# Kernel tuning notes

Hardware: AMD Instinct MI355X
Metric: run time of the kernel (lower is better)

Reference implementation:

```python
import jax, jax.numpy as jnp
import numpy as np

B, S, D, H = 16, 1024, 768, 12
HD = D // H
SCALE = HD ** -0.5


def setup_inputs() -> dict:
    key = jax.random.key(0)
    k1, k2, k3, k4 = jax.random.split(key, 4)
    # Xavier-uniform-like init for the linear weights
    lim_qkv = (6.0 / (D + 3 * D)) ** 0.5
    lim_proj = (6.0 / (D + D)) ** 0.5
    return {
        "hidden_states": jax.random.normal(k1, (B, S, D), dtype=jnp.float32),
        "mask": jax.random.randint(k2, (B, S), 0, 2).astype(bool),
        "qkv_w": jax.random.uniform(k3, (3 * D, D), minval=-lim_qkv, maxval=lim_qkv, dtype=jnp.float32),
        "qkv_b": jnp.zeros((3 * D,), dtype=jnp.float32),
        "proj_w": jax.random.uniform(k4, (D, D), minval=-lim_proj, maxval=lim_proj, dtype=jnp.float32),
        "proj_b": jnp.zeros((D,), dtype=jnp.float32),
    }


def _masked_softmax(scores, attn_mask):
    # scores: [B,H,S,S]; attn_mask: [B,1,S,S] bool. Fully-masked rows -> all-zero
    # weights (torch gives NaN there but then zeroes the output rows; zeroing
    # the weights yields the identical final output without NaNs).
    neg_inf = jnp.finfo(scores.dtype).min
    m = jnp.max(jnp.where(attn_mask, scores, neg_inf), axis=-1, keepdims=True)
    e = jnp.where(attn_mask, jnp.exp(scores - m), 0.0)
    denom = jnp.sum(e, axis=-1, keepdims=True)
    return e / jnp.where(denom == 0, 1.0, denom)


def reference(hidden_states, mask, qkv_w, qkv_b, proj_w, proj_b):
    # fused QKV projection: [B,S,3D]
    qkv = hidden_states @ qkv_w.T + qkv_b
    qkv = qkv.reshape(B, S, 3, H, HD).transpose(2, 0, 3, 1, 4)  # [3,B,H,S,hd]
    q, k, v = qkv[0], qkv[1], qkv[2]
    tok_mask = mask[:, None, :, None]  # [B,1,S,1]
    q = jnp.where(tok_mask, q, 0.0)
    k = jnp.where(tok_mask, k, 0.0)
    v = jnp.where(tok_mask, v, 0.0)
    scores = jnp.einsum("bhqd,bhkd->bhqk", q, k) * SCALE
    attn_mask = (mask[:, :, None] & mask[:, None, :])[:, None]  # [B,1,S,S]
    attn = _masked_softmax(scores, attn_mask)
    context = jnp.einsum("bhqk,bhkd->bhqd", attn, v)
    context = context.transpose(0, 2, 1, 3).reshape(B, S, D)
    out = context @ proj_w.T + proj_b
    out = jnp.where(mask[:, :, None], out, 0.0)
    return out
```

## Files before the change

### kernel.cpp

```cpp
#include <hip/hip_runtime.h>
#include <cstdint>
#include <cstddef>

#define B 16
#define S 1024
#define D 768
#define H 12
#define HD 64
#define NTOK (B * S)
#define QKV_N (3 * D)
#define SCALE 0.125f
#define C2 2.88539008f
#define GK 768
#define NT_K 12

typedef _Float16 f16x8 __attribute__((ext_vector_type(8)));
typedef _Float16 f16x4 __attribute__((ext_vector_type(4)));
typedef __fp16 fp16x2 __attribute__((ext_vector_type(2)));
typedef float f32x4 __attribute__((ext_vector_type(4)));

typedef __attribute__((address_space(3))) void as3_void;
typedef const __attribute__((address_space(1))) void as1_void;

#if defined(__has_builtin)
#if __has_builtin(__builtin_amdgcn_exp2f)
#define EXP2(x) __builtin_amdgcn_exp2f(x)
#else
#define EXP2(x) exp2f(x)
#endif
#else
#define EXP2(x) exp2f(x)
#endif

__global__ __launch_bounds__(256) void normalize_mask_kernel(
    const unsigned char* __restrict__ raw, int* __restrict__ outm, int n) {
    __shared__ int s_isbyte;
    const int tid = threadIdx.x;
    if (tid == 0) s_isbyte = 0;
    __syncthreads();
    int found = 0;
    for (int i = tid; i < n; i += 256) {
        if ((i & 3) != 0 && raw[i] != 0) found = 1;
    }
    if (found) atomicOr(&s_isbyte, 1);
    __syncthreads();
    const int isbyte = s_isbyte;
    if (isbyte) {
        for (int i = tid; i < n; i += 256) outm[i] = raw[i] ? 1 : 0;
    } else {
        const int* r32 = (const int*)raw;
        for (int i = tid; i < n; i += 256) outm[i] = r32[i] ? 1 : 0;
    }
}

__global__ __launch_bounds__(256) void cvt_all_f16(
    const float* __restrict__ in0, _Float16* __restrict__ out0, int n0,
    const float* __restrict__ in1, _Float16* __restrict__ out1, int n1,
    const float* __restrict__ in2, _Float16* __restrict__ out2, int n2) {
    int i = blockIdx.x * 256 + threadIdx.x;
    const float* in;
    _Float16* out;
    if (i < n0) { in = in0; out = out0; }
    else if (i < n0 + n1) { i -= n0; in = in1; out = out1; }
    else { i -= n0 + n1; in = in2; out = out2; if (i >= n2) return; }
    const float4 v = ((const float4*)in)[i];
    f16x4 o;
    o[0] = (_Float16)v.x; o[1] = (_Float16)v.y;
    o[2] = (_Float16)v.z; o[3] = (_Float16)v.w;
    ((f16x4*)out)[i] = o;
}

template <int MODE>
__global__ __launch_bounds__(256, 2) void gemm16(
    const _Float16* __restrict__ A, const _Float16* __restrict__ Wm,
    const float* __restrict__ bias, const int* __restrict__ rowmask,
    int N, float* __restrict__ outf, _Float16* __restrict__ outh,
    _Float16* __restrict__ vtb) {
    __shared__ _Float16 smem[32768];

    const int tid = threadIdx.x;
    const int w = tid >> 6, l = tid & 63;
    const int wm = (w >> 1) * 64, wn = (w & 1) * 64;
    const int lg = l >> 4, lc = l & 15;

    const int bid = blockIdx.x;
    const int xcd = bid & 7;
    const int idx = bid >> 3;
    const int bn = (idx >> 4) * 128;
    const int bm = (xcd * 16 + (idx & 15)) * 128;

    f32x4 acc[4][4] = {};

#define STAGE(T, BUF)                                                           \
    {                                                                           \
        const int kt_ = (T) * 64;                                               \
        _Pragma("unroll")                                                       \
        for (int i_ = 0; i_ < 4; ++i_) {                                        \
            const int ci_ = (w << 2) + i_;                           \
            const int r_ = (ci_ << 3) + (l >> 3);                               \
            const int c16_ = (l & 7) ^ (r_ & 7);                                \
            __builtin_amdgcn_global_load_lds(                                   \
                (as1_void*)(A + (size_t)(bm + r_) * GK + kt_ + c16_ * 8),       \
                (as3_void*)(smem + (BUF) * 8192 + ci_ * 512), 16, 0, 0);        \
            __builtin_amdgcn_global_load_lds(                                   \
                (as1_void*)(Wm + (size_t)(bn + r_) * GK + kt_ + c16_ * 8),      \
                (as3_void*)(smem + 16384 + (BUF) * 8192 + ci_ * 512), 16, 0, 0);\
        }                                                                       \
    }

    STAGE(0, 0)

    for (int t = 0; t < NT_K; ++t) {
        const int cur = t & 1;
        if (t + 1 < NT_K) {
            STAGE(t + 1, cur ^ 1)
            asm volatile("s_waitcnt vmcnt(8)" ::: "memory");
        } else {
            asm volatile("s_waitcnt vmcnt(0)" ::: "memory");
        }
        __builtin_amdgcn_s_barrier();

        const _Float16* sA = smem + cur * 8192;
        const _Float16* sB = smem + 16384 + cur * 8192;
        __builtin_amdgcn_s_setprio(1);
#pragma unroll
        for (int kk = 0; kk < 2; ++kk) {
            const int c16 = ((kk << 2) + lg) ^ (lc & 7);
            f16x8 af[4], bf[4];
#pragma unroll
            for (int ni = 0; ni < 4; ++ni)
                bf[ni] = *(const f16x8*)&sB[(wn + ni * 16 + lc) * 64 + c16 * 8];
#pragma unroll
            for (int mi = 0; mi < 4; ++mi)
                af[mi] = *(const f16x8*)&sA[(wm + mi * 16 + lc) * 64 + c16 * 8];
#pragma unroll
            for (int mi = 0; mi < 4; ++mi)
#pragma unroll
                for (int ni = 0; ni < 4; ++ni)
                    acc[mi][ni] = __builtin_amdgcn_mfma_f32_16x16x32_f16(
                        af[mi], bf[ni], acc[mi][ni], 0, 0, 0);
        }
        __builtin_amdgcn_s_setprio(0);
        __builtin_amdgcn_s_barrier();
    }
#undef STAGE

    float bs[4];
#pragma unroll
    for (int ni = 0; ni < 4; ++ni) bs[ni] = bias[bn + wn + ni * 16 + lc];

    if (MODE == 1) {
        if (bn < 1536) {
#pragma unroll
            for (int mi = 0; mi < 4; ++mi) {
#pragma unroll
                for (int j = 0; j < 4; ++j) {
                    const int m = bm + wm + mi * 16 + lg * 4 + j;
#pragma unroll
                    for (int ni = 0; ni < 4; ++ni) {
                        const int col = bn + wn + ni * 16 + lc;
                        outh[(size_t)m * N + col] =
                            (_Float16)(acc[mi][ni][j] + bs[ni]);
                    }
                }
            }
        } else {
#pragma unroll
            for (int mi = 0; mi < 4; ++mi) {
#pragma unroll
                for (int ni = 0; ni < 4; ++ni) {
                    f16x4 v4;
#pragma unroll
                    for (int j = 0; j < 4; ++j)
                        v4[j] = (_Float16)(acc[mi][ni][j] + bs[ni]);
                    const int nl = wn + ni * 16 + lc;
                    const int ml = wm + mi * 16 + lg * 4;
                    *(f16x4*)&smem[nl * 136 + ml] = v4;
                }
            }
            __syncthreads();
            const int r = tid >> 1;
            const int c0 = (tid & 1) * 64;
            const int col0 = bn - 1536 + r;
            const int hh = col0 >> 6, hd = col0 & 63;
            const int bb = bm >> 10;
            const int s0 = (bm & 1023) + c0;
            _Float16* dst = vtb + ((size_t)(bb * H + hh) * HD + hd) * S + s0;
#pragma unroll
            for (int e = 0; e < 8; ++e)
                *(f16x8*)(dst + e * 8) = *(const f16x8*)&smem[r * 136 + c0 + e * 8];
        }
    } else {
#pragma unroll
        for (int mi = 0; mi < 4; ++mi) {
#pragma unroll
            for (int j = 0; j < 4; ++j) {
                const int m = bm + wm + mi * 16 + lg * 4 + j;
                const int mv = rowmask[m];
#pragma unroll
                for (int ni = 0; ni < 4; ++ni) {
                    const int col = bn + wn + ni * 16 + lc;
                    outf[(size_t)m * N + col] = mv ? acc[mi][ni][j] + bs[ni] : 0.f;
                }
            }
        }
    }
}

__global__ __launch_bounds__(256) void attn_kernel(
    const _Float16* __restrict__ qkv, const _Float16* __restrict__ vtb,
    const int* __restrict__ mask, _Float16* __restrict__ ctx) {
    __shared__ _Float16 ksm[2][64 * 64];
    __shared__ _Float16 vsm[2][64 * 68];
    __shared__ float mbias[S];

    const int blk = blockIdx.x;
    const int xcd = blk & 7;
    const int idx = blk >> 3;
    const int bh_ = xcd * 24 + (idx >> 3);
    const int qt = idx & 7;
    const int h = bh_ % H;
    const int b = bh_ / H;
    const int tid = threadIdx.x;
    const int w = tid >> 6, lane = tid & 63;
    const int lg = lane >> 4, lc = lane & 15;

    const size_t bh = (size_t)(b * H + h);
    const _Float16* Kp = qkv + (size_t)(b * S) * QKV_N + D + h * HD;
    const _Float16* Vt = vtb + bh * HD * S;
    const int* mrow = mask + b * S;

    const int r0 = w * 8 + (lane >> 3);
    const int s0 = lane & 7;
    const int koff0 = r0 * QKV_N + (s0 ^ (r0 & 7)) * 8;
    const int koff1 = (32 + r0) * QKV_N + (s0 ^ ((32 + r0) & 7)) * 8;
    const int srow = tid >> 3;
    const int scol = (tid & 7) * 8;

#define KSTAGE(KT, BUF)                                                        \
    {                                                                          \
        __builtin_amdgcn_global_load_lds(                                      \
            (as1_void*)(Kp + (size_t)(KT) * QKV_N + koff0),                    \
            (as3_void*)(&ksm[BUF][w * 512]), 16, 0, 0);                        \
        __builtin_amdgcn_global_load_lds(                                      \
            (as1_void*)(Kp + (size_t)(KT) * QKV_N + koff1),                    \
            (as3_void*)(&ksm[BUF][2048 + w * 512]), 16, 0, 0);                 \
    }

    const int qrow0 = qt * 128 + w * 16 + lc;
    const _Float16* Qp0 = qkv + (size_t)(b * S + qrow0) * QKV_N + h * HD;
    const _Float16* Qp1 = Qp0 + (size_t)64 * QKV_N;
    f16x8 qa0 = *(const f16x8*)(Qp0 + lg * 8);
    f16x8 qa1 = *(const f16x8*)(Qp0 + 32 + lg * 8);
    f16x8 qb0 = *(const f16x8*)(Qp1 + lg * 8);
    f16x8 qb1 = *(const f16x8*)(Qp1 + 32 + lg * 8);
    const _Float16 qs = (_Float16)(0.125f * 1.44269504f);
    qa0 *= qs; qa1 *= qs; qb0 *= qs; qb1 *= qs;

#pragma unroll
    for (int i = 0; i < 4; ++i)
        mbias[i * 256 + tid] = mrow[i * 256 + tid] ? -C2 : -1e9f;

    KSTAGE(0, 0)
    {
        const f16x8 gv0 = *(const f16x8*)(Vt + (size_t)srow * S + scol);
        const f16x8 gv1 = *(const f16x8*)(Vt + (size_t)(32 + srow) * S + scol);
        asm volatile("s_waitcnt vmcnt(0)" ::: "memory");
        *(f16x4*)&vsm[0][srow * 68 + scol] = ((const f16x4*)&gv0)[0];
        *(f16x4*)&vsm[0][srow * 68 + scol + 4] = ((const f16x4*)&gv0)[1];
        *(f16x4*)&vsm[0][(32 + srow) * 68 + scol] = ((const f16x4*)&gv1)[0];
        *(f16x4*)&vsm[0][(32 + srow) * 68 + scol + 4] = ((const f16x4*)&gv1)[1];
    }
    __syncthreads();

    f32x4 acca[4] = {}, accb[4] = {};
    float l_a = 0.f, l_b = 0.f;
    fp16x2 ones;
    ones[0] = (__fp16)1.0f; ones[1] = (__fp16)1.0f;

    for (int it = 0; it < S / 64; ++it) {
        const int cur = it & 1;
        const int ktn = (it + 1) * 64;
        const bool pref = (it + 1 < S / 64);
        f16x8 gv0, gv1;
        if (pref) {
            KSTAGE(ktn, cur ^ 1)
            gv0 = *(const f16x8*)(Vt + (size_t)srow * S + ktn + scol);
            gv1 = *(const f16x8*)(Vt + (size_t)(32 + srow) * S + ktn + scol);
        }

        __builtin_amdgcn_s_setprio(1);
#pragma unroll
        for (int t = 0; t < 4; ++t) {
            const int krow = (t * 16 + lc) * 64;
            const f16x8 kfa =
                *(const f16x8*)&ksm[cur][krow + (lg ^ (lc & 7)) * 8];
            const f16x8 kfb =
                *(const f16x8*)&ksm[cur][krow + ((4 + lg) ^ (lc & 7)) * 8];
            const f32x4 mb = *(const f32x4*)&mbias[it * 64 + t * 16 + 4 * lg];

            f32x4 ca = mb, cb = mb;
            ca = __builtin_amdgcn_mfma_f32_16x16x32_f16(kfa, qa0, ca, 0, 0, 0);
            ca = __builtin_amdgcn_mfma_f32_16x16x32_f16(kfb, qa1, ca, 0, 0, 0);
            cb = __builtin_amdgcn_mfma_f32_16x16x32_f16(kfa, qb0, cb, 0, 0, 0);
            cb = __builtin_amdgcn_mfma_f32_16x16x32_f16(kfb, qb1, cb, 0, 0, 0);

            const auto ua0 = __builtin_amdgcn_cvt_pkrtz(EXP2(ca[0]), EXP2(ca[1]));
            const auto ua1 = __builtin_amdgcn_cvt_pkrtz(EXP2(ca[2]), EXP2(ca[3]));
            const auto ub0 = __builtin_amdgcn_cvt_pkrtz(EXP2(cb[0]), EXP2(cb[1]));
            const auto ub1 = __builtin_amdgcn_cvt_pkrtz(EXP2(cb[2]), EXP2(cb[3]));
            l_a = __builtin_amdgcn_fdot2(ua0, ones, l_a, false);
            l_a = __builtin_amdgcn_fdot2(ua1, ones, l_a, false);
            l_b = __builtin_amdgcn_fdot2(ub0, ones, l_b, false);
            l_b = __builtin_amdgcn_fdot2(ub1, ones, l_b, false);

            f16x4 pa, pb;
            pa[0] = (_Float16)ua0[0]; pa[1] = (_Float16)ua0[1];
            pa[2] = (_Float16)ua1[0]; pa[3] = (_Float16)ua1[1];
            pb[0] = (_Float16)ub0[0]; pb[1] = (_Float16)ub0[1];
            pb[2] = (_Float16)ub1[0]; pb[3] = (_Float16)ub1[1];

#pragma unroll
            for (int g = 0; g < 4; ++g) {
                const f16x4 vf =
                    *(const f16x4*)&vsm[cur][(g * 16 + lc) * 68 + t * 16 + lg * 4];
                acca[g] = __builtin_amdgcn_mfma_f32_16x16x16f16(pa, vf, acca[g], 0, 0, 0);
                accb[g] = __builtin_amdgcn_mfma_f32_16x16x16f16(pb, vf, accb[g], 0, 0, 0);
            }
        }
        __builtin_amdgcn_s_setprio(0);

        if (pref) {
            asm volatile("s_waitcnt vmcnt(0)" ::: "memory");
            *(f16x4*)&vsm[cur ^ 1][srow * 68 + scol] = ((const f16x4*)&gv0)[0];
            *(f16x4*)&vsm[cur ^ 1][srow * 68 + scol + 4] = ((const f16x4*)&gv0)[1];
            *(f16x4*)&vsm[cur ^ 1][(32 + srow) * 68 + scol] = ((const f16x4*)&gv1)[0];
            *(f16x4*)&vsm[cur ^ 1][(32 + srow) * 68 + scol + 4] = ((const f16x4*)&gv1)[1];
        }
        __syncthreads();
    }
#undef KSTAGE

    float la = l_a, lb = l_b;
    la += __shfl_xor(la, 16); la += __shfl_xor(la, 32);
    lb += __shfl_xor(lb, 16); lb += __shfl_xor(lb, 32);
    const float inva = la > 0.f ? 1.f / la : 0.f;
    const float invb = lb > 0.f ? 1.f / lb : 0.f;

#pragma unroll
    for (int j = 0; j < 4; ++j) {
        const int qin = 4 * lg + j;
        const float ija = __shfl(inva, qin);
        const float ijb = __shfl(invb, qin);
        const int qra = qt * 128 + w * 16 + qin;
        const int qrb = qra + 64;
        const float iqa = mrow[qra] ? ija : 0.f;
        const float iqb = mrow[qrb] ? ijb : 0.f;
        const size_t oa = ((size_t)(b * S + qra)) * D + h * HD;
        const size_t ob = ((size_t)(b * S + qrb)) * D + h * HD;
#pragma unroll
        for (int g = 0; g < 4; ++g) {
            ctx[oa + 16 * g + lc] = (_Float16)(acca[g][j] * iqa);
            ctx[ob + 16 * g + lc] = (_Float16)(accb[g][j] * iqb);
        }
    }
}

extern "C" void kernel_launch(void* const* d_in, const int* in_sizes, int n_in,
                              void* d_out, int out_size, void* d_ws, size_t ws_size,
                              hipStream_t stream) {
    const float* hidden = (const float*)d_in[0];
    const unsigned char* maskraw = (const unsigned char*)d_in[1];
    const float* qkv_w = (const float*)d_in[2];
    const float* qkv_b = (const float*)d_in[3];
    const float* proj_w = (const float*)d_in[4];
    const float* proj_b = (const float*)d_in[5];
    float* out = (float*)d_out;

    char* ws = (char*)d_ws;
    size_t off = 0;
    int* maskN = (int*)(ws + off);            off += (size_t)NTOK * 4;
    _Float16* hid16 = (_Float16*)(ws + off);  off += (size_t)NTOK * D * 2;
    _Float16* qkvw16 = (_Float16*)(ws + off); off += (size_t)QKV_N * D * 2;
    _Float16* projw16 = (_Float16*)(ws + off); off += (size_t)D * D * 2;
    _Float16* qkv16 = (_Float16*)(ws + off);  off += (size_t)NTOK * QKV_N * 2;
    _Float16* vt = (_Float16*)(ws + off);     off += (size_t)NTOK * D * 2;
    _Float16* ctx16 = (_Float16*)(ws + off);  off += (size_t)NTOK * D * 2;

    normalize_mask_kernel<<<1, 256, 0, stream>>>(maskraw, maskN, NTOK);

    const int n0 = NTOK * D / 4, n1 = QKV_N * D / 4, n2 = D * D / 4;
    cvt_all_f16<<<(n0 + n1 + n2 + 255) / 256, 256, 0, stream>>>(
        hidden, hid16, n0, qkv_w, qkvw16, n1, proj_w, projw16, n2);

    gemm16<1><<<dim3(2304), 256, 0, stream>>>(
        hid16, qkvw16, qkv_b, nullptr, QKV_N, nullptr, qkv16, vt);

    attn_kernel<<<dim3(B * H * (S / 128)), 256, 0, stream>>>(qkv16, vt, maskN, ctx16);

    gemm16<0><<<dim3(768), 256, 0, stream>>>(
        ctx16, projw16, proj_b, maskN, D, out, nullptr, nullptr);
}
```

Measured before the change: 207.7 us.

## Double attention query tile per block and stage V via async LDS loads

Each attention block now handles 256 query rows (4 groups of 64 per wave set) instead of 128, so every K/V tile loaded into shared memory is reused across twice as many queries and the grid halves. V tiles are now staged with global_load_lds directly into an XOR-swizzled 64-wide layout, like K, replacing register round-trips, the padded 68 stride and the explicit vmcnt wait. Launch bounds request 3 blocks per CU, which raises register pressure given the larger accumulator set (16 f32x4 accumulators plus 8 Q fragments) and risks spills or lower occupancy. Fewer blocks (768) may also reduce load balance across CUs.

```diff
diff --git a/kernel.cpp b/kernel.cpp
--- a/kernel.cpp
+++ b/kernel.cpp
@@ -207,18 +207,18 @@
     }
 }
 
-__global__ __launch_bounds__(256) void attn_kernel(
+__global__ __launch_bounds__(256, 3) void attn_kernel(
     const _Float16* __restrict__ qkv, const _Float16* __restrict__ vtb,
     const int* __restrict__ mask, _Float16* __restrict__ ctx) {
     __shared__ _Float16 ksm[2][64 * 64];
-    __shared__ _Float16 vsm[2][64 * 68];
+    __shared__ _Float16 vsm[2][64 * 64];
     __shared__ float mbias[S];
 
     const int blk = blockIdx.x;
     const int xcd = blk & 7;
     const int idx = blk >> 3;
-    const int bh_ = xcd * 24 + (idx >> 3);
-    const int qt = idx & 7;
+    const int bh_ = xcd * 24 + (idx >> 2);
+    const int qt = idx & 3;
     const int h = bh_ % H;
     const int b = bh_ / H;
     const int tid = threadIdx.x;
@@ -231,13 +231,13 @@
     const int* mrow = mask + b * S;
 
     const int r0 = w * 8 + (lane >> 3);
-    const int s0 = lane & 7;
-    const int koff0 = r0 * QKV_N + (s0 ^ (r0 & 7)) * 8;
-    const int koff1 = (32 + r0) * QKV_N + (s0 ^ ((32 + r0) & 7)) * 8;
-    const int srow = tid >> 3;
-    const int scol = (tid & 7) * 8;
-
-#define KSTAGE(KT, BUF)                                                        \
+    const int swz8 = ((lane & 7) ^ (r0 & 7)) * 8;
+    const int koff0 = r0 * QKV_N + swz8;
+    const int koff1 = (32 + r0) * QKV_N + swz8;
+    const int voff0 = r0 * S + swz8;
+    const int voff1 = (32 + r0) * S + swz8;
+
+#define STAGE(KT, BUF)                                                         \
     {                                                                          \
         __builtin_amdgcn_global_load_lds(                                      \
             (as1_void*)(Kp + (size_t)(KT) * QKV_N + koff0),                    \
@@ -245,49 +245,42 @@
         __builtin_amdgcn_global_load_lds(                                      \
             (as1_void*)(Kp + (size_t)(KT) * QKV_N + koff1),                    \
             (as3_void*)(&ksm[BUF][2048 + w * 512]), 16, 0, 0);                 \
-    }
-
-    const int qrow0 = qt * 128 + w * 16 + lc;
-    const _Float16* Qp0 = qkv + (size_t)(b * S + qrow0) * QKV_N + h * HD;
-    const _Float16* Qp1 = Qp0 + (size_t)64 * QKV_N;
-    f16x8 qa0 = *(const f16x8*)(Qp0 + lg * 8);
-    f16x8 qa1 = *(const f16x8*)(Qp0 + 32 + lg * 8);
-    f16x8 qb0 = *(const f16x8*)(Qp1 + lg * 8);
-    f16x8 qb1 = *(const f16x8*)(Qp1 + 32 + lg * 8);
+        __builtin_amdgcn_global_load_lds(                                      \
+            (as1_void*)(Vt + (size_t)(KT) + voff0),                            \
+            (as3_void*)(&vsm[BUF][w * 512]), 16, 0, 0);                        \
+        __builtin_amdgcn_global_load_lds(                                      \
+            (as1_void*)(Vt + (size_t)(KT) + voff1),                            \
+            (as3_void*)(&vsm[BUF][2048 + w * 512]), 16, 0, 0);                 \
+    }
+
+    const int qbase = qt * 256 + w * 16 + lc;
     const _Float16 qs = (_Float16)(0.125f * 1.44269504f);
-    qa0 *= qs; qa1 *= qs; qb0 *= qs; qb1 *= qs;
+    f16x8 qf[4][2];
+#pragma unroll
+    for (int qg = 0; qg < 4; ++qg) {
+        const _Float16* Qp =
+            qkv + (size_t)(b * S + qbase + qg * 64) * QKV_N + h * HD;
+        qf[qg][0] = *(const f16x8*)(Qp + lg * 8);
+        qf[qg][1] = *(const f16x8*)(Qp + 32 + lg * 8);
+        qf[qg][0] *= qs;
+        qf[qg][1] *= qs;
+    }
 
 #pragma unroll
     for (int i = 0; i < 4; ++i)
         mbias[i * 256 + tid] = mrow[i * 256 + tid] ? -C2 : -1e9f;
 
-    KSTAGE(0, 0)
-    {
-        const f16x8 gv0 = *(const f16x8*)(Vt + (size_t)srow * S + scol);
-        const f16x8 gv1 = *(const f16x8*)(Vt + (size_t)(32 + srow) * S + scol);
-        asm volatile("s_waitcnt vmcnt(0)" ::: "memory");
-        *(f16x4*)&vsm[0][srow * 68 + scol] = ((const f16x4*)&gv0)[0];
-        *(f16x4*)&vsm[0][srow * 68 + scol + 4] = ((const f16x4*)&gv0)[1];
-        *(f16x4*)&vsm[0][(32 + srow) * 68 + scol] = ((const f16x4*)&gv1)[0];
-        *(f16x4*)&vsm[0][(32 + srow) * 68 + scol + 4] = ((const f16x4*)&gv1)[1];
-    }
+    STAGE(0, 0)
     __syncthreads();
 
-    f32x4 acca[4] = {}, accb[4] = {};
-    float l_a = 0.f, l_b = 0.f;
+    f32x4 acc[4][4] = {};
+    float lsum[4] = {0.f, 0.f, 0.f, 0.f};
     fp16x2 ones;
     ones[0] = (__fp16)1.0f; ones[1] = (__fp16)1.0f;
 
     for (int it = 0; it < S / 64; ++it) {
         const int cur = it & 1;
-        const int ktn = (it + 1) * 64;
-        const bool pref = (it + 1 < S / 64);
-        f16x8 gv0, gv1;
-        if (pref) {
-            KSTAGE(ktn, cur ^ 1)
-            gv0 = *(const f16x8*)(Vt + (size_t)srow * S + ktn + scol);
-            gv1 = *(const f16x8*)(Vt + (size_t)(32 + srow) * S + ktn + scol);
-        }
+        if (it + 1 < S / 64) STAGE((it + 1) * 64, cur ^ 1)
 
         __builtin_amdgcn_s_setprio(1);
 #pragma unroll
@@ -299,69 +292,52 @@
                 *(const f16x8*)&ksm[cur][krow + ((4 + lg) ^ (lc & 7)) * 8];
             const f32x4 mb = *(const f32x4*)&mbias[it * 64 + t * 16 + 4 * lg];
 
-            f32x4 ca = mb, cb = mb;
-            ca = __builtin_amdgcn_mfma_f32_16x16x32_f16(kfa, qa0, ca, 0, 0, 0);
-            ca = __builtin_amdgcn_mfma_f32_16x16x32_f16(kfb, qa1, ca, 0, 0, 0);
-            cb = __builtin_amdgcn_mfma_f32_16x16x32_f16(kfa, qb0, cb, 0, 0, 0);
-            cb = __builtin_amdgcn_mfma_f32_16x16x32_f16(kfb, qb1, cb, 0, 0, 0);
-
-            const auto ua0 = __builtin_amdgcn_cvt_pkrtz(EXP2(ca[0]), EXP2(ca[1]));
-            const auto ua1 = __builtin_amdgcn_cvt_pkrtz(EXP2(ca[2]), EXP2(ca[3]));
-            const auto ub0 = __builtin_amdgcn_cvt_pkrtz(EXP2(cb[0]), EXP2(cb[1]));
-            const auto ub1 = __builtin_amdgcn_cvt_pkrtz(EXP2(cb[2]), EXP2(cb[3]));
-            l_a = __builtin_amdgcn_fdot2(ua0, ones, l_a, false);
-            l_a = __builtin_amdgcn_fdot2(ua1, ones, l_a, false);
-            l_b = __builtin_amdgcn_fdot2(ub0, ones, l_b, false);
-            l_b = __builtin_amdgcn_fdot2(ub1, ones, l_b, false);
-
-            f16x4 pa, pb;
-            pa[0] = (_Float16)ua0[0]; pa[1] = (_Float16)ua0[1];
-            pa[2] = (_Float16)ua1[0]; pa[3] = (_Float16)ua1[1];
-            pb[0] = (_Float16)ub0[0]; pb[1] = (_Float16)ub0[1];
-            pb[2] = (_Float16)ub1[0]; pb[3] = (_Float16)ub1[1];
+            f16x4 pp[4];
+#pragma unroll
+            for (int qg = 0; qg < 4; ++qg) {
+                f32x4 c = mb;
+                c = __builtin_amdgcn_mfma_f32_16x16x32_f16(kfa, qf[qg][0], c, 0, 0, 0);
+                c = __builtin_amdgcn_mfma_f32_16x16x32_f16(kfb, qf[qg][1], c, 0, 0, 0);
+                const auto u0 = __builtin_amdgcn_cvt_pkrtz(EXP2(c[0]), EXP2(c[1]));
+                const auto u1 = __builtin_amdgcn_cvt_pkrtz(EXP2(c[2]), EXP2(c[3]));
+                lsum[qg] = __builtin_amdgcn_fdot2(u0, ones, lsum[qg], false);
+                lsum[qg] = __builtin_amdgcn_fdot2(u1, ones, lsum[qg], false);
+                pp[qg][0] = (_Float16)u0[0]; pp[qg][1] = (_Float16)u0[1];
+                pp[qg][2] = (_Float16)u1[0]; pp[qg][3] = (_Float16)u1[1];
+            }
 
 #pragma unroll
             for (int g = 0; g < 4; ++g) {
-                const f16x4 vf =
-                    *(const f16x4*)&vsm[cur][(g * 16 + lc) * 68 + t * 16 + lg * 4];
-                acca[g] = __builtin_amdgcn_mfma_f32_16x16x16f16(pa, vf, acca[g], 0, 0, 0);
-                accb[g] = __builtin_amdgcn_mfma_f32_16x16x16f16(pb, vf, accb[g], 0, 0, 0);
+                const int vrow = (g * 16 + lc) * 64;
+                const f16x4 vf = *(const f16x4*)&vsm[cur][
+                    vrow + (((2 * t + (lg >> 1)) ^ (lc & 7)) << 3) + (lg & 1) * 4];
+#pragma unroll
+                for (int qg = 0; qg < 4; ++qg)
+                    acc[qg][g] = __builtin_amdgcn_mfma_f32_16x16x16f16(
+                        pp[qg], vf, acc[qg][g], 0, 0, 0);
             }
         }
         __builtin_amdgcn_s_setprio(0);
-
-        if (pref) {
-            asm volatile("s_waitcnt vmcnt(0)" ::: "memory");
-            *(f16x4*)&vsm[cur ^ 1][srow * 68 + scol] = ((const f16x4*)&gv0)[0];
-            *(f16x4*)&vsm[cur ^ 1][srow * 68 + scol + 4] = ((const f16x4*)&gv0)[1];
-            *(f16x4*)&vsm[cur ^ 1][(32 + srow) * 68 + scol] = ((const f16x4*)&gv1)[0];
-            *(f16x4*)&vsm[cur ^ 1][(32 + srow) * 68 + scol + 4] = ((const f16x4*)&gv1)[1];
-        }
         __syncthreads();
     }
-#undef KSTAGE
-
-    float la = l_a, lb = l_b;
-    la += __shfl_xor(la, 16); la += __shfl_xor(la, 32);
-    lb += __shfl_xor(lb, 16); lb += __shfl_xor(lb, 32);
-    const float inva = la > 0.f ? 1.f / la : 0.f;
-    const float invb = lb > 0.f ? 1.f / lb : 0.f;
-
-#pragma unroll
-    for (int j = 0; j < 4; ++j) {
-        const int qin = 4 * lg + j;
-        const float ija = __shfl(inva, qin);
-        const float ijb = __shfl(invb, qin);
-        const int qra = qt * 128 + w * 16 + qin;
-        const int qrb = qra + 64;
-        const float iqa = mrow[qra] ? ija : 0.f;
-        const float iqb = mrow[qrb] ? ijb : 0.f;
-        const size_t oa = ((size_t)(b * S + qra)) * D + h * HD;
-        const size_t ob = ((size_t)(b * S + qrb)) * D + h * HD;
-#pragma unroll
-        for (int g = 0; g < 4; ++g) {
-            ctx[oa + 16 * g + lc] = (_Float16)(acca[g][j] * iqa);
-            ctx[ob + 16 * g + lc] = (_Float16)(accb[g][j] * iqb);
+#undef STAGE
+
+#pragma unroll
+    for (int qg = 0; qg < 4; ++qg) {
+        float l = lsum[qg];
+        l += __shfl_xor(l, 16);
+        l += __shfl_xor(l, 32);
+        const float inv = l > 0.f ? 1.f / l : 0.f;
+#pragma unroll
+        for (int j = 0; j < 4; ++j) {
+            const int qin = 4 * lg + j;
+            const float ij = __shfl(inv, qin);
+            const int qr = qt * 256 + qg * 64 + w * 16 + qin;
+            const float iq = mrow[qr] ? ij : 0.f;
+            const size_t o = ((size_t)(b * S + qr)) * D + h * HD;
+#pragma unroll
+            for (int g = 0; g < 4; ++g)
+                ctx[o + 16 * g + lc] = (_Float16)(acc[qg][g][j] * iq);
         }
     }
 }
@@ -396,7 +372,7 @@
     gemm16<1><<<dim3(2304), 256, 0, stream>>>(
         hid16, qkvw16, qkv_b, nullptr, QKV_N, nullptr, qkv16, vt);
 
-    attn_kernel<<<dim3(B * H * (S / 128)), 256, 0, stream>>>(qkv16, vt, maskN, ctx16);
+    attn_kernel<<<dim3(B * H * (S / 256)), 256, 0, stream>>>(qkv16, vt, maskN, ctx16);
 
     gemm16<0><<<dim3(768), 256, 0, stream>>>(
         ctx16, projw16, proj_b, maskN, D, out, nullptr, nullptr);
```

Result: no change. 206.7 us (-0.4%).
